# Optimization experiments

Hardware: AMD Instinct MI355X
Metric: run time of the kernel (lower is better)

## Reference

```python
import jax, jax.numpy as jnp
import numpy as np

N = 8192        # nodes
E = 49152       # edges (~avg degree 6, triangular mesh)
H = 6           # GATv2 heads
C = 512         # hidden_size (per-head out channels)
F_IN = 2 + C    # GATv2 in_channels = coord(2) + hidden(512)
ALL_FEAT = 37   # deform_in_c-2 + 16 + 16
NUM_LOOP = 3
LRELU_SLOPE = 0.2


def setup_inputs() -> dict:
    key = jax.random.key(0)
    ks = jax.random.split(key, 10)
    x = jax.random.uniform(ks[0], (N, 7), dtype=jnp.float32)
    local_feat = jax.random.normal(ks[1], (N, 16), dtype=jnp.float32)
    conv_feat = jax.random.normal(ks[2], (N, 16), dtype=jnp.float32)
    edge_index = jax.random.randint(ks[3], (2, E), 0, N, dtype=jnp.int64)
    bd_mask = jnp.zeros((N,), jnp.int32)  # poly_mesh=False path
    W_lin = jax.random.normal(ks[4], (ALL_FEAT, C), dtype=jnp.float32) / np.float32(np.sqrt(ALL_FEAT))
    b_lin = jnp.zeros((C,), jnp.float32)
    Wl = jax.random.normal(ks[5], (F_IN, H * C), dtype=jnp.float32) / np.float32(np.sqrt(F_IN))
    Wr = jax.random.normal(ks[6], (F_IN, H * C), dtype=jnp.float32) / np.float32(np.sqrt(F_IN))
    att = jax.random.normal(ks[7], (H, C), dtype=jnp.float32) / np.float32(np.sqrt(C))
    gat_bias = jnp.zeros((C,), jnp.float32)
    W_coord = jax.random.normal(ks[8], (C, 2), dtype=jnp.float32) / np.float32(np.sqrt(C))
    b_coord = jnp.zeros((2,), jnp.float32)
    return dict(x=x, local_feat=local_feat, conv_feat=conv_feat,
                W_lin=W_lin, b_lin=b_lin, Wl=Wl, Wr=Wr, att=att,
                gat_bias=gat_bias, W_coord=W_coord, b_coord=b_coord,
                edge_index=edge_index, bd_mask=bd_mask)


def _gatv2(feat, src, dst, Wl, Wr, att, bias):
    # PyG GATv2Conv: lin_l on source, lin_r on target, additive attention
    n = feat.shape[0]
    xl = (feat @ Wl).reshape(n, H, C)            # source-side transform
    xr = (feat @ Wr).reshape(n, H, C)            # target-side transform
    e = xl[src] + xr[dst]                        # [E', H, C]
    e = jax.nn.leaky_relu(e, LRELU_SLOPE)
    logits = jnp.einsum('ehc,hc->eh', e, att)    # [E', H]
    m = jax.ops.segment_max(logits, dst, num_segments=n)
    m = jnp.where(jnp.isfinite(m), m, 0.0)
    a = jnp.exp(logits - m[dst])
    denom = jax.ops.segment_sum(a, dst, num_segments=n) + 1e-16
    alpha = a / denom[dst]                       # segment softmax over incoming edges
    msg = xl[src] * alpha[:, :, None]            # [E', H, C]
    out = jax.ops.segment_sum(msg, dst, num_segments=n)  # [N, H, C]
    return out.mean(axis=1) + bias               # concat=False -> mean over heads


def reference(x, local_feat, conv_feat, W_lin, b_lin, Wl, Wr, att, gat_bias,
              W_coord, b_coord, edge_index, bd_mask):
    coord = x[:, :2]
    hidden_in = jnp.concatenate([x[:, 2:], local_feat, conv_feat], axis=1)
    hidden = jax.nn.selu(hidden_in @ W_lin + b_lin)
    # GATv2Conv adds self-loops by default
    loops = jnp.arange(N, dtype=edge_index.dtype)
    src = jnp.concatenate([edge_index[0], loops])
    dst = jnp.concatenate([edge_index[1], loops])
    for _ in range(NUM_LOOP):
        up = coord[:, 0] == 1.0
        down = coord[:, 0] == 0.0
        left = coord[:, 1] == 0.0
        right = coord[:, 1] == 1.0
        feat = jnp.concatenate([coord, hidden], axis=1)   # [N, 514]
        hidden = jax.nn.selu(_gatv2(feat, src, dst, Wl, Wr, att, gat_bias))
        out = hidden @ W_coord + b_coord                  # [N, 2]
        ox = jnp.where(down, 0.0, jnp.where(up, 1.0, out[:, 0]))
        oy = jnp.where(right, 1.0, jnp.where(left, 0.0, out[:, 1]))
        coord = jnp.stack([ox, oy], axis=1)
    return coord
```

## Files before the change

### kernel.cpp

```cpp
#include <hip/hip_runtime.h>
#include <hip/hip_bf16.h>
#include <math.h>

#define N_NODES   8192
#define NUM_E     49152
#define NUM_EDGES (NUM_E + N_NODES)
#define H_HEADS   6
#define C_DIM     512
#define HC        (H_HEADS * C_DIM)
#define XLR       (2 * HC)
#define N_FEAT    37
#define LRELU_SLOPE 0.2f
#define SELU_LAMBDA 1.0507009873554805f
#define SELU_ALPHA  1.6732632423543772f

typedef __bf16 bf16_t;
typedef bf16_t bf16x8 __attribute__((ext_vector_type(8)));
typedef float  f32x4  __attribute__((ext_vector_type(4)));
typedef float  f32x2  __attribute__((ext_vector_type(2)));

__device__ __forceinline__ int edge_src(const int* ei, int e) {
    return e < NUM_E ? ei[e] : (e - NUM_E);
}
__device__ __forceinline__ int edge_dst(const int* ei, int e) {
    return e < NUM_E ? ei[NUM_E + e] : (e - NUM_E);
}
__device__ __forceinline__ float selu_f(float v) {
    return v > 0.f ? SELU_LAMBDA * v : SELU_LAMBDA * SELU_ALPHA * (__expf(v) - 1.f);
}
__device__ __forceinline__ void gload_lds16(const void* g, void* l) {
    __builtin_amdgcn_global_load_lds((const __attribute__((address_space(1))) void*)g,
                                     (__attribute__((address_space(3))) void*)l, 16, 0, 0);
}

__global__ __launch_bounds__(512) void k_hidden0(
    const float* __restrict__ x, const float* __restrict__ lf,
    const float* __restrict__ cf, const float* __restrict__ W,
    const float* __restrict__ b, bf16_t* __restrict__ hidden,
    float* __restrict__ coord)
{
    int n0 = blockIdx.x * 4;
    int c = threadIdx.x;
    __shared__ float f[4][N_FEAT];
    if (c < 4 * N_FEAT) {
        int m = c / N_FEAT, k = c - m * N_FEAT;
        int n = n0 + m;
        f[m][k] = (k < 5) ? x[n*7 + 2 + k]
                 : (k < 21 ? lf[n*16 + (k - 5)] : cf[n*16 + (k - 21)]);
    }
    if (c < 8) coord[n0*2 + c] = x[(n0 + (c >> 1))*7 + (c & 1)];
    __syncthreads();
    float a0 = b[c], a1 = a0, a2 = a0, a3 = a0;
    #pragma unroll
    for (int k = 0; k < N_FEAT; ++k) {
        float wv = W[k*C_DIM + c];
        a0 = fmaf(f[0][k], wv, a0);
        a1 = fmaf(f[1][k], wv, a1);
        a2 = fmaf(f[2][k], wv, a2);
        a3 = fmaf(f[3][k], wv, a3);
    }
    hidden[(size_t)(n0 + 0)*C_DIM + c] = (bf16_t)selu_f(a0);
    hidden[(size_t)(n0 + 1)*C_DIM + c] = (bf16_t)selu_f(a1);
    hidden[(size_t)(n0 + 2)*C_DIM + c] = (bf16_t)selu_f(a2);
    hidden[(size_t)(n0 + 3)*C_DIM + c] = (bf16_t)selu_f(a3);
}

__global__ __launch_bounds__(256) void k_wt_transpose(const float* __restrict__ W,
                                                      bf16_t* __restrict__ WT)
{
    __shared__ float tile[32][33];
    int k0 = blockIdx.y * 32;
    int n0 = blockIdx.x * 32;
    int tx = threadIdx.x & 31, ty = threadIdx.x >> 5;
    #pragma unroll
    for (int i = 0; i < 4; ++i)
        tile[ty + i*8][tx] = W[(size_t)(k0 + 2 + ty + i*8) * HC + n0 + tx];
    __syncthreads();
    #pragma unroll
    for (int i = 0; i < 4; ++i)
        WT[(size_t)(n0 + ty + i*8) * C_DIM + k0 + tx] = (bf16_t)tile[tx][ty + i*8];
}

__global__ void k_hist(const int* __restrict__ ei, int* __restrict__ counts) {
    int e = blockIdx.x * blockDim.x + threadIdx.x;
    if (e >= NUM_EDGES) return;
    atomicAdd(&counts[edge_dst(ei, e)], 1);
}

__global__ __launch_bounds__(256) void k_scan(const int* __restrict__ counts,
                                              int* __restrict__ row_ptr,
                                              int* __restrict__ cursor) {
    __shared__ int part[256];
    __shared__ int off[257];
    int t = threadIdx.x;
    int base = t * 32;
    int local[32];
    int s = 0;
    #pragma unroll
    for (int i = 0; i < 32; ++i) { local[i] = s; s += counts[base + i]; }
    part[t] = s;
    __syncthreads();
    if (t == 0) {
        off[0] = 0;
        for (int i = 0; i < 256; ++i) off[i+1] = off[i] + part[i];
    }
    __syncthreads();
    int o = off[t];
    #pragma unroll
    for (int i = 0; i < 32; ++i) {
        int v = o + local[i];
        row_ptr[base + i] = v;
        cursor[base + i]  = v;
    }
    if (t == 255) row_ptr[N_NODES] = off[256];
}

__global__ void k_scatter(const int* __restrict__ ei, int* __restrict__ cursor,
                          int* __restrict__ csr_src) {
    int e = blockIdx.x * blockDim.x + threadIdx.x;
    if (e >= NUM_EDGES) return;
    int pos = atomicAdd(&cursor[edge_dst(ei, e)], 1);
    csr_src[pos] = edge_src(ei, e);
}

#define BM 256
#define BN 256
#define BK 64
#define NT (C_DIM / BK)
#define NBX (XLR / BN)
#define NWG ((N_NODES / BM) * NBX)

__global__ __launch_bounds__(512, 2) void k_gemm_bf16(
    const bf16_t* __restrict__ A,
    const bf16_t* __restrict__ BT,
    const float*  __restrict__ Wl,
    const float*  __restrict__ Wr,
    const float*  __restrict__ coord,
    bf16_t* __restrict__ out)
{
    __shared__ __align__(1024) char smem[131072];
    char* sA = smem;
    char* sB = smem + 65536;

    const int tid  = threadIdx.x;
    const int wave = tid >> 6;
    const int lane = tid & 63;
    const int wm   = wave >> 2;
    const int wn   = wave & 3;

    int bid = blockIdx.y * gridDim.x + blockIdx.x;
    bid = (bid & 7) * (NWG / 8) + (bid >> 3);
    const int rowBase = (bid / NBX) * BM;
    const int colBase = (bid % NBX) * BN;

    const int rtid = tid >> 3;
    const int csw  = ((tid & 7) * 8) ^ (((tid >> 3) & 7) << 3);
    const bf16_t* pA = A  + (size_t)(rowBase + rtid) * C_DIM + csw;
    const bf16_t* pB = BT + (size_t)(colBase + rtid) * C_DIM + csw;

    auto stageA = [&](int t, int h) {
        char* l = sA + ((t & 1) << 15) + (h << 14) + (wave << 10);
        const bf16_t* g = pA + (size_t)(h * 128) * C_DIM + t * BK;
        gload_lds16(g,              l);
        gload_lds16(g + 64 * C_DIM, l + 8192);
    };
    auto stageB = [&](int t, int h) {
        char* l = sB + ((t & 1) << 15) + (h << 14) + (wave << 10);
        const bf16_t* g = pB + (size_t)(h * 128) * C_DIM + t * BK;
        gload_lds16(g,              l);
        gload_lds16(g + 64 * C_DIM, l + 8192);
    };

    stageB(0, 0); stageB(0, 1); stageA(0, 0); stageA(0, 1);
    stageB(1, 0); stageB(1, 1);
    __builtin_amdgcn_sched_barrier(0);
    asm volatile("s_waitcnt vmcnt(4)" ::: "memory");
    __builtin_amdgcn_sched_barrier(0);
    __builtin_amdgcn_s_barrier();
    __builtin_amdgcn_sched_barrier(0);

    const int kb  = (lane >> 4) << 4;
    const int sw  = (lane & 7) << 4;
    const int xt0 = kb ^ sw;
    const int xt1 = (64 | kb) ^ sw;
    const int aRowOff = (wm * 128 + (lane & 15)) * 128;
    const int bRowOff = (wn * 64  + (lane & 15)) * 128;

    f32x4 acc[8][4] = {};

    #pragma unroll 2
    for (int t = 0; t < NT; ++t) {
        const char* aP = sA + ((t & 1) << 15) + aRowOff;
        const char* bP = sB + ((t & 1) << 15) + bRowOff;
        bf16x8 bfv[4][2];

        #pragma unroll
        for (int ph = 0; ph < 4; ++ph) {
            if (ph == 0)      { if (t + 1 < NT) stageA(t + 1, 0); }
            else if (ph == 1) { if (t + 1 < NT) stageA(t + 1, 1); }
            else if (ph == 2) { if (t + 2 < NT) stageB(t + 2, 0); }
            else              { if (t + 2 < NT) stageB(t + 2, 1); }

            if (ph == 0) {
                #pragma unroll
                for (int nf = 0; nf < 4; ++nf) {
                    bfv[nf][0] = *(const bf16x8*)(bP + nf * 2048 + xt0);
                    bfv[nf][1] = *(const bf16x8*)(bP + nf * 2048 + xt1);
                }
            }
            bf16x8 af0k0 = *(const bf16x8*)(aP + (2*ph)     * 2048 + xt0);
            bf16x8 af0k1 = *(const bf16x8*)(aP + (2*ph)     * 2048 + xt1);
            bf16x8 af1k0 = *(const bf16x8*)(aP + (2*ph + 1) * 2048 + xt0);
            bf16x8 af1k1 = *(const bf16x8*)(aP + (2*ph + 1) * 2048 + xt1);

            __builtin_amdgcn_s_setprio(1);
            #pragma unroll
            for (int nf = 0; nf < 4; ++nf) {
                acc[2*ph  ][nf] = __builtin_amdgcn_mfma_f32_16x16x32_bf16(af0k0, bfv[nf][0], acc[2*ph  ][nf], 0, 0, 0);
                acc[2*ph+1][nf] = __builtin_amdgcn_mfma_f32_16x16x32_bf16(af1k0, bfv[nf][0], acc[2*ph+1][nf], 0, 0, 0);
            }
            #pragma unroll
            for (int nf = 0; nf < 4; ++nf) {
                acc[2*ph  ][nf] = __builtin_amdgcn_mfma_f32_16x16x32_bf16(af0k1, bfv[nf][1], acc[2*ph  ][nf], 0, 0, 0);
                acc[2*ph+1][nf] = __builtin_amdgcn_mfma_f32_16x16x32_bf16(af1k1, bfv[nf][1], acc[2*ph+1][nf], 0, 0, 0);
            }
            __builtin_amdgcn_s_setprio(0);

            if (ph == 3) {
                __builtin_amdgcn_sched_barrier(0);
                if (t < NT - 2)       asm volatile("s_waitcnt vmcnt(4)" ::: "memory");
                else if (t == NT - 2) asm volatile("s_waitcnt vmcnt(0)" ::: "memory");
            }
            __builtin_amdgcn_sched_barrier(0);
            asm volatile("s_waitcnt lgkmcnt(0)" ::: "memory");
            __builtin_amdgcn_s_barrier();
            __builtin_amdgcn_sched_barrier(0);
        }
    }

    const float* Wtop = (colBase < HC) ? Wl : Wr;
    const int coff = (colBase < HC) ? 0 : HC;
    const int ccol  = lane & 15;
    const int crow4 = (lane >> 4) * 4;

    float wv0[4], wv1[4];
    #pragma unroll
    for (int nf = 0; nf < 4; ++nf) {
        int wcol = colBase + wn*64 + nf*16 + ccol - coff;
        wv0[nf] = Wtop[wcol];
        wv1[nf] = Wtop[HC + wcol];
    }
    #pragma unroll
    for (int mf = 0; mf < 8; ++mf) {
        #pragma unroll
        for (int r = 0; r < 4; ++r) {
            int row = rowBase + wm*128 + mf*16 + crow4 + r;
            float c0 = coord[row*2 + 0], c1 = coord[row*2 + 1];
            size_t rb = (size_t)row * XLR;
            #pragma unroll
            for (int nf = 0; nf < 4; ++nf) {
                int col = colBase + wn*64 + nf*16 + ccol;
                out[rb + col] = (bf16_t)(acc[mf][nf][r] + c0 * wv0[nf] + c1 * wv1[nf]);
            }
        }
    }
}

#define MAX_DEG 128
__global__ __launch_bounds__(384) void k_attn_agg(
    const bf16_t* __restrict__ xlr,
    const int* __restrict__ row_ptr, const int* __restrict__ csr_src,
    const float* __restrict__ att,
    const float* __restrict__ gat_bias, const float* __restrict__ W_coord,
    const float* __restrict__ b_coord, const float* __restrict__ coord_in,
    bf16_t* __restrict__ hidden, float* __restrict__ coord_out)
{
    int n = blockIdx.x;
    int tid = threadIdx.x;
    int h = tid >> 6, lane = tid & 63;
    __shared__ int   s_src[MAX_DEG];
    __shared__ float s_acc[HC];
    __shared__ float s_red[12];

    int beg = row_ptr[n];
    int deg = min(row_ptr[n + 1] - beg, MAX_DEG);
    for (int j = tid; j < deg; j += 384) s_src[j] = csr_src[beg + j];
    __syncthreads();

    size_t off = (size_t)h * C_DIM + lane * 8;
    bf16x8 xrv = *(const bf16x8*)(xlr + (size_t)n * XLR + HC + off);
    f32x2 xr2[4], at2[4], ac2[4] = {};
    #pragma unroll
    for (int i = 0; i < 4; ++i) {
        xr2[i] = f32x2{(float)xrv[2*i], (float)xrv[2*i+1]};
        at2[i] = f32x2{att[off + 2*i], att[off + 2*i + 1]};
    }

    float l = 0.f;
    int j = 0;
    for (; j + 2 <= deg; j += 2) {
        bf16x8 xa = *(const bf16x8*)(xlr + (size_t)s_src[j]     * XLR + off);
        bf16x8 xb = *(const bf16x8*)(xlr + (size_t)s_src[j + 1] * XLR + off);
        f32x2 xla[4], xlb[4];
        #pragma unroll
        for (int i = 0; i < 4; ++i) {
            xla[i] = f32x2{(float)xa[2*i], (float)xa[2*i+1]};
            xlb[i] = f32x2{(float)xb[2*i], (float)xb[2*i+1]};
        }
        f32x2 sa = {0.f, 0.f}, sb = {0.f, 0.f};
        #pragma unroll
        for (int i = 0; i < 4; ++i) {
            f32x2 va = xla[i] + xr2[i];
            f32x2 vb = xlb[i] + xr2[i];
            sa += __builtin_elementwise_max(va, va * LRELU_SLOPE) * at2[i];
            sb += __builtin_elementwise_max(vb, vb * LRELU_SLOPE) * at2[i];
        }
        float suma = sa.x + sa.y, sumb = sb.x + sb.y;
        #pragma unroll
        for (int o = 1; o < 64; o <<= 1) {
            suma += __shfl_xor(suma, o);
            sumb += __shfl_xor(sumb, o);
        }
        float aa = __expf(suma), ab = __expf(sumb);
        l += aa + ab;
        #pragma unroll
        for (int i = 0; i < 4; ++i) ac2[i] += aa * xla[i] + ab * xlb[i];
    }
    if (j < deg) {
        bf16x8 xa = *(const bf16x8*)(xlr + (size_t)s_src[j] * XLR + off);
        f32x2 xla[4];
        #pragma unroll
        for (int i = 0; i < 4; ++i) xla[i] = f32x2{(float)xa[2*i], (float)xa[2*i+1]};
        f32x2 sa = {0.f, 0.f};
        #pragma unroll
        for (int i = 0; i < 4; ++i) {
            f32x2 va = xla[i] + xr2[i];
            sa += __builtin_elementwise_max(va, va * LRELU_SLOPE) * at2[i];
        }
        float suma = sa.x + sa.y;
        #pragma unroll
        for (int o = 1; o < 64; o <<= 1) suma += __shfl_xor(suma, o);
        float aa = __expf(suma);
        l += aa;
        #pragma unroll
        for (int i = 0; i < 4; ++i) ac2[i] += aa * xla[i];
    }

    float invl = 1.f / (l + 1e-16f) * (1.f / 6.f);
    #pragma unroll
    for (int i = 0; i < 4; ++i) {
        s_acc[off + 2*i]     = ac2[i].x * invl;
        s_acc[off + 2*i + 1] = ac2[i].y * invl;
    }
    __syncthreads();

    float p0 = 0.f, p1 = 0.f;
    for (int c = tid; c < C_DIM; c += 384) {
        float s = 0.f;
        #pragma unroll
        for (int hh = 0; hh < H_HEADS; ++hh) s += s_acc[hh * C_DIM + c];
        float hv = selu_f(s + gat_bias[c]);
        hidden[n * C_DIM + c] = (bf16_t)hv;
        p0 = fmaf(hv, W_coord[c * 2 + 0], p0);
        p1 = fmaf(hv, W_coord[c * 2 + 1], p1);
    }
    #pragma unroll
    for (int o = 32; o > 0; o >>= 1) { p0 += __shfl_down(p0, o); p1 += __shfl_down(p1, o); }
    if (lane == 0) { s_red[h * 2] = p0; s_red[h * 2 + 1] = p1; }
    __syncthreads();
    if (tid == 0) {
        float o0 = b_coord[0], o1 = b_coord[1];
        #pragma unroll
        for (int w = 0; w < H_HEADS; ++w) { o0 += s_red[w * 2]; o1 += s_red[w * 2 + 1]; }
        float cx = coord_in[n * 2 + 0], cy = coord_in[n * 2 + 1];
        float ox = (cx == 0.0f) ? 0.f : ((cx == 1.0f) ? 1.f : o0);
        float oy = (cy == 1.0f) ? 1.f : ((cy == 0.0f) ? 0.f : o1);
        coord_out[n * 2 + 0] = ox;
        coord_out[n * 2 + 1] = oy;
    }
}

extern "C" void kernel_launch(void* const* d_in, const int* in_sizes, int n_in,
                              void* d_out, int out_size, void* d_ws, size_t ws_size,
                              hipStream_t stream)
{
    const float* x       = (const float*)d_in[0];
    const float* lf      = (const float*)d_in[1];
    const float* cf      = (const float*)d_in[2];
    const float* W_lin   = (const float*)d_in[3];
    const float* b_lin   = (const float*)d_in[4];
    const float* Wl      = (const float*)d_in[5];
    const float* Wr      = (const float*)d_in[6];
    const float* att     = (const float*)d_in[7];
    const float* gbias   = (const float*)d_in[8];
    const float* W_coord = (const float*)d_in[9];
    const float* b_coord = (const float*)d_in[10];
    const int*   ei      = (const int*)d_in[11];

    char* w = (char*)d_ws;
    auto alloc = [&](size_t bytes) { char* p = w; w += (bytes + 255) & ~255ull; return p; };
    bf16_t*   hidden  = (bf16_t*)alloc((size_t)N_NODES * C_DIM * 2);
    bf16_t*   WT      = (bf16_t*)alloc((size_t)XLR * C_DIM * 2);
    bf16_t*   xlr     = (bf16_t*)alloc((size_t)N_NODES * XLR * 2);
    int*      counts  = (int*)alloc((size_t)N_NODES * 4);
    int*      row_ptr = (int*)alloc((size_t)(N_NODES + 1) * 4);
    int*      cursor  = (int*)alloc((size_t)N_NODES * 4);
    int*      csr_src = (int*)alloc((size_t)NUM_EDGES * 4);
    float*    cA      = (float*)alloc((size_t)N_NODES * 2 * 4);
    float*    cB      = (float*)alloc((size_t)N_NODES * 2 * 4);

    hipMemsetAsync(counts, 0, (size_t)N_NODES * 4, stream);
    k_hidden0<<<N_NODES / 4, 512, 0, stream>>>(x, lf, cf, W_lin, b_lin, hidden, cA);
    {
        dim3 tg(HC / 32, C_DIM / 32);
        k_wt_transpose<<<tg, 256, 0, stream>>>(Wl, WT);
        k_wt_transpose<<<tg, 256, 0, stream>>>(Wr, WT + (size_t)HC * C_DIM);
    }
    k_hist<<<(NUM_EDGES + 255) / 256, 256, 0, stream>>>(ei, counts);
    k_scan<<<1, 256, 0, stream>>>(counts, row_ptr, cursor);
    k_scatter<<<(NUM_EDGES + 255) / 256, 256, 0, stream>>>(ei, cursor, csr_src);

    float* cin = cA;
    for (int it = 0; it < 3; ++it) {
        float* cout = (it == 2) ? (float*)d_out : ((it == 0) ? cB : cA);
        dim3 g(NBX, N_NODES / BM);
        k_gemm_bf16<<<g, 512, 0, stream>>>(hidden, WT, Wl, Wr, cin, xlr);
        k_attn_agg<<<N_NODES, 384, 0, stream>>>(xlr, row_ptr, csr_src, att,
                                                gbias, W_coord, b_coord, cin, hidden, cout);
        cin = cout;
    }
}
```

Before: 554.7 us.

## Prefetch next A fragments from LDS one phase ahead in GEMM main loop

Restructures the bf16 MFMA GEMM loop so A-operand LDS reads for the next phase (and the first phase of the next K-tile) are issued before the current phase's MFMAs, with partial lgkmcnt waits instead of a full drain each phase. The global-load vmcnt wait is moved earlier in phase 3 so the next tile's first A fragments can be read before the barrier. It also adds a min-blocks hint to the attention aggregation kernel's launch bounds, which can cap its register use. The aim is to hide LDS latency behind MFMA work, at the cost of more live registers and more delicate wait-count ordering.

```diff
diff --git a/kernel.cpp b/kernel.cpp
--- a/kernel.cpp
+++ b/kernel.cpp
@@ -176,8 +176,6 @@
     __builtin_amdgcn_sched_barrier(0);
     asm volatile("s_waitcnt vmcnt(4)" ::: "memory");
     __builtin_amdgcn_sched_barrier(0);
-    __builtin_amdgcn_s_barrier();
-    __builtin_amdgcn_sched_barrier(0);
 
     const int kb  = (lane >> 4) << 4;
     const int sw  = (lane & 7) << 4;
@@ -186,12 +184,25 @@
     const int aRowOff = (wm * 128 + (lane & 15)) * 128;
     const int bRowOff = (wn * 64  + (lane & 15)) * 128;
 
+    bf16x8 af[2][2][2];
+    {
+        const char* aP0 = sA + aRowOff;
+        af[0][0][0] = *(const bf16x8*)(aP0 + 0*2048 + xt0);
+        af[0][0][1] = *(const bf16x8*)(aP0 + 0*2048 + xt1);
+        af[0][1][0] = *(const bf16x8*)(aP0 + 1*2048 + xt0);
+        af[0][1][1] = *(const bf16x8*)(aP0 + 1*2048 + xt1);
+    }
+    __builtin_amdgcn_sched_barrier(0);
+    __builtin_amdgcn_s_barrier();
+    __builtin_amdgcn_sched_barrier(0);
+
     f32x4 acc[8][4] = {};
 
     #pragma unroll 2
     for (int t = 0; t < NT; ++t) {
-        const char* aP = sA + ((t & 1) << 15) + aRowOff;
-        const char* bP = sB + ((t & 1) << 15) + bRowOff;
+        const char* aP  = sA + ((t & 1) << 15) + aRowOff;
+        const char* bP  = sB + ((t & 1) << 15) + bRowOff;
+        const char* aPn = sA + (((t + 1) & 1) << 15) + aRowOff;
         bf16x8 bfv[4][2];
 
         #pragma unroll
@@ -200,6 +211,13 @@
             else if (ph == 1) { if (t + 1 < NT) stageA(t + 1, 1); }
             else if (ph == 2) { if (t + 2 < NT) stageB(t + 2, 0); }
             else              { if (t + 2 < NT) stageB(t + 2, 1); }
+
+            if (ph == 3) {
+                __builtin_amdgcn_sched_barrier(0);
+                if (t < NT - 2)       asm volatile("s_waitcnt vmcnt(4)" ::: "memory");
+                else if (t == NT - 2) asm volatile("s_waitcnt vmcnt(0)" ::: "memory");
+                __builtin_amdgcn_sched_barrier(0);
+            }
 
             if (ph == 0) {
                 #pragma unroll
@@ -207,32 +225,51 @@
                     bfv[nf][0] = *(const bf16x8*)(bP + nf * 2048 + xt0);
                     bfv[nf][1] = *(const bf16x8*)(bP + nf * 2048 + xt1);
                 }
+                af[1][0][0] = *(const bf16x8*)(aP + 2*2048 + xt0);
+                af[1][0][1] = *(const bf16x8*)(aP + 2*2048 + xt1);
+                af[1][1][0] = *(const bf16x8*)(aP + 3*2048 + xt0);
+                af[1][1][1] = *(const bf16x8*)(aP + 3*2048 + xt1);
+                asm volatile("s_waitcnt lgkmcnt(0)" ::: "memory");
+            } else if (ph == 1) {
+                af[0][0][0] = *(const bf16x8*)(aP + 4*2048 + xt0);
+                af[0][0][1] = *(const bf16x8*)(aP + 4*2048 + xt1);
+                af[0][1][0] = *(const bf16x8*)(aP + 5*2048 + xt0);
+                af[0][1][1] = *(const bf16x8*)(aP + 5*2048 + xt1);
+                asm volatile("s_waitcnt lgkmcnt(4)" ::: "memory");
+            } else if (ph == 2) {
+                af[1][0][0] = *(const bf16x8*)(aP + 6*2048 + xt0);
+                af[1][0][1] = *(const bf16x8*)(aP + 6*2048 + xt1);
+                af[1][1][0] = *(const bf16x8*)(aP + 7*2048 + xt0);
+                af[1][1][1] = *(const bf16x8*)(aP + 7*2048 + xt1);
+                asm volatile("s_waitcnt lgkmcnt(4)" ::: "memory");
+            } else {
+                if (t + 1 < NT) {
+                    af[0][0][0] = *(const bf16x8*)(aPn + 0*2048 + xt0);
+                    af[0][0][1] = *(const bf16x8*)(aPn + 0*2048 + xt1);
+                    af[0][1][0] = *(const bf16x8*)(aPn + 1*2048 + xt0);
+                    af[0][1][1] = *(const bf16x8*)(aPn + 1*2048 + xt1);
+                    asm volatile("s_waitcnt lgkmcnt(4)" ::: "memory");
+                } else {
+                    asm volatile("s_waitcnt lgkmcnt(0)" ::: "memory");
+                }
             }
-            bf16x8 af0k0 = *(const bf16x8*)(aP + (2*ph)     * 2048 + xt0);
-            bf16x8 af0k1 = *(const bf16x8*)(aP + (2*ph)     * 2048 + xt1);
-            bf16x8 af1k0 = *(const bf16x8*)(aP + (2*ph + 1) * 2048 + xt0);
-            bf16x8 af1k1 = *(const bf16x8*)(aP + (2*ph + 1) * 2048 + xt1);
-
+            __builtin_amdgcn_sched_barrier(0);
+
+            const int p2 = ph & 1;
             __builtin_amdgcn_s_setprio(1);
             #pragma unroll
             for (int nf = 0; nf < 4; ++nf) {
-                acc[2*ph  ][nf] = __builtin_amdgcn_mfma_f32_16x16x32_bf16(af0k0, bfv[nf][0], acc[2*ph  ][nf], 0, 0, 0);
-                acc[2*ph+1][nf] = __builtin_amdgcn_mfma_f32_16x16x32_bf16(af1k0, bfv[nf][0], acc[2*ph+1][nf], 0, 0, 0);
+                acc[2*ph  ][nf] = __builtin_amdgcn_mfma_f32_16x16x32_bf16(af[p2][0][0], bfv[nf][0], acc[2*ph  ][nf], 0, 0, 0);
+                acc[2*ph+1][nf] = __builtin_amdgcn_mfma_f32_16x16x32_bf16(af[p2][1][0], bfv[nf][0], acc[2*ph+1][nf], 0, 0, 0);
             }
             #pragma unroll
             for (int nf = 0; nf < 4; ++nf) {
-                acc[2*ph  ][nf] = __builtin_amdgcn_mfma_f32_16x16x32_bf16(af0k1, bfv[nf][1], acc[2*ph  ][nf], 0, 0, 0);
-                acc[2*ph+1][nf] = __builtin_amdgcn_mfma_f32_16x16x32_bf16(af1k1, bfv[nf][1], acc[2*ph+1][nf], 0, 0, 0);
+                acc[2*ph  ][nf] = __builtin_amdgcn_mfma_f32_16x16x32_bf16(af[p2][0][1], bfv[nf][1], acc[2*ph  ][nf], 0, 0, 0);
+                acc[2*ph+1][nf] = __builtin_amdgcn_mfma_f32_16x16x32_bf16(af[p2][1][1], bfv[nf][1], acc[2*ph+1][nf], 0, 0, 0);
             }
             __builtin_amdgcn_s_setprio(0);
 
-            if (ph == 3) {
-                __builtin_amdgcn_sched_barrier(0);
-                if (t < NT - 2)       asm volatile("s_waitcnt vmcnt(4)" ::: "memory");
-                else if (t == NT - 2) asm volatile("s_waitcnt vmcnt(0)" ::: "memory");
-            }
             __builtin_amdgcn_sched_barrier(0);
-            asm volatile("s_waitcnt lgkmcnt(0)" ::: "memory");
             __builtin_amdgcn_s_barrier();
             __builtin_amdgcn_sched_barrier(0);
         }
@@ -267,7 +304,7 @@
 }
 
 #define MAX_DEG 128
-__global__ __launch_bounds__(384) void k_attn_agg(
+__global__ __launch_bounds__(384, 8) void k_attn_agg(
     const bf16_t* __restrict__ xlr,
     const int* __restrict__ row_ptr, const int* __restrict__ csr_src,
     const float* __restrict__ att,
```

Measured after the change: 540.1 us. 1.03x faster.

## Halve GEMM barriers per k-tile and use DPP butterfly reductions in attention

Applied to the files above, without the earlier changes.

The GEMM main loop drops from four phases per k-tile, each ending in a barrier, to two halves that each load four A fragments and issue 32 MFMAs, so there are two barriers per tile instead of four. The attention kernel replaces its 64-lane shfl_xor reduction with DPP row operations plus ds_swizzle and a single cross-half shuffle, which avoids most LDS-backed permutes. It also adds an occupancy hint to launch_bounds. The GEMM change holds more A fragments in registers and overlaps fewer loads with compute, which may raise register pressure and expose LDS latency.

```diff
diff --git a/kernel.cpp b/kernel.cpp
--- a/kernel.cpp
+++ b/kernel.cpp
@@ -31,6 +31,21 @@
 __device__ __forceinline__ void gload_lds16(const void* g, void* l) {
     __builtin_amdgcn_global_load_lds((const __attribute__((address_space(1))) void*)g,
                                      (__attribute__((address_space(3))) void*)l, 16, 0, 0);
+}
+
+__device__ __forceinline__ float bfly_add64(float s) {
+    int t;
+    t = __builtin_amdgcn_update_dpp(0, __float_as_int(s), 0xB1,  0xF, 0xF, true);
+    s += __int_as_float(t);
+    t = __builtin_amdgcn_update_dpp(0, __float_as_int(s), 0x4E,  0xF, 0xF, true);
+    s += __int_as_float(t);
+    t = __builtin_amdgcn_update_dpp(0, __float_as_int(s), 0x141, 0xF, 0xF, true);
+    s += __int_as_float(t);
+    t = __builtin_amdgcn_update_dpp(0, __float_as_int(s), 0x140, 0xF, 0xF, true);
+    s += __int_as_float(t);
+    s += __int_as_float(__builtin_amdgcn_ds_swizzle(__float_as_int(s), 0x401F));
+    s += __shfl_xor(s, 32);
+    return s;
 }
 
 __global__ __launch_bounds__(512) void k_hidden0(
@@ -176,7 +191,7 @@
     __builtin_amdgcn_sched_barrier(0);
     asm volatile("s_waitcnt vmcnt(4)" ::: "memory");
     __builtin_amdgcn_sched_barrier(0);
-    __builtin_amdgcn_s_barrier();
+    asm volatile("s_barrier" ::: "memory");
     __builtin_amdgcn_sched_barrier(0);
 
     const int kb  = (lane >> 4) << 4;
@@ -193,49 +208,59 @@
         const char* aP = sA + ((t & 1) << 15) + aRowOff;
         const char* bP = sB + ((t & 1) << 15) + bRowOff;
         bf16x8 bfv[4][2];
-
-        #pragma unroll
-        for (int ph = 0; ph < 4; ++ph) {
-            if (ph == 0)      { if (t + 1 < NT) stageA(t + 1, 0); }
-            else if (ph == 1) { if (t + 1 < NT) stageA(t + 1, 1); }
-            else if (ph == 2) { if (t + 2 < NT) stageB(t + 2, 0); }
-            else              { if (t + 2 < NT) stageB(t + 2, 1); }
-
-            if (ph == 0) {
-                #pragma unroll
-                for (int nf = 0; nf < 4; ++nf) {
-                    bfv[nf][0] = *(const bf16x8*)(bP + nf * 2048 + xt0);
-                    bfv[nf][1] = *(const bf16x8*)(bP + nf * 2048 + xt1);
-                }
-            }
-            bf16x8 af0k0 = *(const bf16x8*)(aP + (2*ph)     * 2048 + xt0);
-            bf16x8 af0k1 = *(const bf16x8*)(aP + (2*ph)     * 2048 + xt1);
-            bf16x8 af1k0 = *(const bf16x8*)(aP + (2*ph + 1) * 2048 + xt0);
-            bf16x8 af1k1 = *(const bf16x8*)(aP + (2*ph + 1) * 2048 + xt1);
-
-            __builtin_amdgcn_s_setprio(1);
+        bf16x8 af[4][2];
+
+        if (t + 1 < NT) { stageA(t + 1, 0); stageA(t + 1, 1); }
+        #pragma unroll
+        for (int mf = 0; mf < 4; ++mf) {
+            af[mf][0] = *(const bf16x8*)(aP + mf*2048 + xt0);
+            af[mf][1] = *(const bf16x8*)(aP + mf*2048 + xt1);
+        }
+        #pragma unroll
+        for (int nf = 0; nf < 4; ++nf) {
+            bfv[nf][0] = *(const bf16x8*)(bP + nf * 2048 + xt0);
+            bfv[nf][1] = *(const bf16x8*)(bP + nf * 2048 + xt1);
+        }
+        __builtin_amdgcn_s_setprio(1);
+        #pragma unroll
+        for (int nf = 0; nf < 4; ++nf)
             #pragma unroll
-            for (int nf = 0; nf < 4; ++nf) {
-                acc[2*ph  ][nf] = __builtin_amdgcn_mfma_f32_16x16x32_bf16(af0k0, bfv[nf][0], acc[2*ph  ][nf], 0, 0, 0);
-                acc[2*ph+1][nf] = __builtin_amdgcn_mfma_f32_16x16x32_bf16(af1k0, bfv[nf][0], acc[2*ph+1][nf], 0, 0, 0);
-            }
+            for (int mf = 0; mf < 4; ++mf)
+                acc[mf][nf] = __builtin_amdgcn_mfma_f32_16x16x32_bf16(af[mf][0], bfv[nf][0], acc[mf][nf], 0, 0, 0);
+        #pragma unroll
+        for (int nf = 0; nf < 4; ++nf)
             #pragma unroll
-            for (int nf = 0; nf < 4; ++nf) {
-                acc[2*ph  ][nf] = __builtin_amdgcn_mfma_f32_16x16x32_bf16(af0k1, bfv[nf][1], acc[2*ph  ][nf], 0, 0, 0);
-                acc[2*ph+1][nf] = __builtin_amdgcn_mfma_f32_16x16x32_bf16(af1k1, bfv[nf][1], acc[2*ph+1][nf], 0, 0, 0);
-            }
-            __builtin_amdgcn_s_setprio(0);
-
-            if (ph == 3) {
-                __builtin_amdgcn_sched_barrier(0);
-                if (t < NT - 2)       asm volatile("s_waitcnt vmcnt(4)" ::: "memory");
-                else if (t == NT - 2) asm volatile("s_waitcnt vmcnt(0)" ::: "memory");
-            }
-            __builtin_amdgcn_sched_barrier(0);
-            asm volatile("s_waitcnt lgkmcnt(0)" ::: "memory");
-            __builtin_amdgcn_s_barrier();
-            __builtin_amdgcn_sched_barrier(0);
-        }
+            for (int mf = 0; mf < 4; ++mf)
+                acc[mf][nf] = __builtin_amdgcn_mfma_f32_16x16x32_bf16(af[mf][1], bfv[nf][1], acc[mf][nf], 0, 0, 0);
+        __builtin_amdgcn_s_setprio(0);
+        __builtin_amdgcn_sched_barrier(0);
+        asm volatile("s_barrier" ::: "memory");
+        __builtin_amdgcn_sched_barrier(0);
+
+        if (t + 2 < NT) { stageB(t + 2, 0); stageB(t + 2, 1); }
+        #pragma unroll
+        for (int mf = 0; mf < 4; ++mf) {
+            af[mf][0] = *(const bf16x8*)(aP + (4 + mf)*2048 + xt0);
+            af[mf][1] = *(const bf16x8*)(aP + (4 + mf)*2048 + xt1);
+        }
+        __builtin_amdgcn_s_setprio(1);
+        #pragma unroll
+        for (int nf = 0; nf < 4; ++nf)
+            #pragma unroll
+            for (int mf = 0; mf < 4; ++mf)
+                acc[4 + mf][nf] = __builtin_amdgcn_mfma_f32_16x16x32_bf16(af[mf][0], bfv[nf][0], acc[4 + mf][nf], 0, 0, 0);
+        #pragma unroll
+        for (int nf = 0; nf < 4; ++nf)
+            #pragma unroll
+            for (int mf = 0; mf < 4; ++mf)
+                acc[4 + mf][nf] = __builtin_amdgcn_mfma_f32_16x16x32_bf16(af[mf][1], bfv[nf][1], acc[4 + mf][nf], 0, 0, 0);
+        __builtin_amdgcn_s_setprio(0);
+        __builtin_amdgcn_sched_barrier(0);
+        if (t < NT - 2)       asm volatile("s_waitcnt vmcnt(4)" ::: "memory");
+        else if (t == NT - 2) asm volatile("s_waitcnt vmcnt(0)" ::: "memory");
+        __builtin_amdgcn_sched_barrier(0);
+        asm volatile("s_barrier" ::: "memory");
+        __builtin_amdgcn_sched_barrier(0);
     }
 
     const float* Wtop = (colBase < HC) ? Wl : Wr;
@@ -267,7 +292,7 @@
 }
 
 #define MAX_DEG 128
-__global__ __launch_bounds__(384) void k_attn_agg(
+__global__ __launch_bounds__(384, 8) void k_attn_agg(
     const bf16_t* __restrict__ xlr,
     const int* __restrict__ row_ptr, const int* __restrict__ csr_src,
     const float* __restrict__ att,
@@ -315,12 +340,8 @@
             sa += __builtin_elementwise_max(va, va * LRELU_SLOPE) * at2[i];
             sb += __builtin_elementwise_max(vb, vb * LRELU_SLOPE) * at2[i];
         }
-        float suma = sa.x + sa.y, sumb = sb.x + sb.y;
-        #pragma unroll
-        for (int o = 1; o < 64; o <<= 1) {
-            suma += __shfl_xor(suma, o);
-            sumb += __shfl_xor(sumb, o);
-        }
+        float suma = bfly_add64(sa.x + sa.y);
+        float sumb = bfly_add64(sb.x + sb.y);
         float aa = __expf(suma), ab = __expf(sumb);
         l += aa + ab;
         #pragma unroll
@@ -337,9 +358,7 @@
             f32x2 va = xla[i] + xr2[i];
             sa += __builtin_elementwise_max(va, va * LRELU_SLOPE) * at2[i];
         }
-        float suma = sa.x + sa.y;
-        #pragma unroll
-        for (int o = 1; o < 64; o <<= 1) suma += __shfl_xor(suma, o);
+        float suma = bfly_add64(sa.x + sa.y);
         float aa = __expf(suma);
         l += aa;
         #pragma unroll
```

After: 484.1 us. 12.7% less time.
